# Optimization experiments

Measured on AMD Instinct MI355X. Metric: run time of the kernel, lower is better.

## Reference

```python
import jax, jax.numpy as jnp
import numpy as np

H1 = 51  # lstm1 hidden size
H2 = 1   # lstm2 hidden size


def _lstm_cell(x, h, c, Wih, Whh, bih, bhh):
    # PyTorch LSTMCell: gates = x W_ih^T + b_ih + h W_hh^T + b_hh, order i,f,g,o
    gates = x @ Wih.T + h @ Whh.T + (bih + bhh)
    i, f, g, o = jnp.split(gates, 4, axis=-1)
    i = jax.nn.sigmoid(i)
    f = jax.nn.sigmoid(f)
    g = jnp.tanh(g)
    o = jax.nn.sigmoid(o)
    c_new = f * c + i * g
    h_new = o * jnp.tanh(c_new)
    return h_new, c_new


def setup_inputs() -> dict:
    key = jax.random.key(0)
    ks = jax.random.split(key, 9)
    B, T = 2048, 1024
    s1 = 1.0 / np.sqrt(H1)
    s2 = 1.0 / np.sqrt(H2)
    u = lambda k, shape, s: jax.random.uniform(k, shape, jnp.float32, -s, s)
    return {
        "input": jax.random.normal(ks[0], (B, T), dtype=jnp.float32),
        "W_ih1": u(ks[1], (4 * H1, 1), s1),
        "W_hh1": u(ks[2], (4 * H1, H1), s1),
        "b_ih1": u(ks[3], (4 * H1,), s1),
        "b_hh1": u(ks[4], (4 * H1,), s1),
        "W_ih2": u(ks[5], (4 * H2, H1), s2),
        "W_hh2": u(ks[6], (4 * H2, H2), s2),
        "b_ih2": u(ks[7], (4 * H2,), s2),
        "b_hh2": u(ks[8], (4 * H2,), s2),
        "future": 64,
    }


def reference(input, W_ih1, W_hh1, b_ih1, b_hh1, W_ih2, W_hh2, b_ih2, b_hh2, future):
    B = input.shape[0]
    dt = input.dtype
    h1 = jnp.zeros((B, H1), dt)
    c1 = jnp.zeros((B, H1), dt)
    h2 = jnp.zeros((B, H2), dt)
    c2 = jnp.zeros((B, H2), dt)

    def step(carry, x_t):
        h1, c1, h2, c2 = carry
        h1, c1 = _lstm_cell(x_t, h1, c1, W_ih1, W_hh1, b_ih1, b_hh1)
        h2, c2 = _lstm_cell(h1, h2, c2, W_ih2, W_hh2, b_ih2, b_hh2)
        return (h1, c1, h2, c2), h2

    xs = jnp.swapaxes(input, 0, 1)[:, :, None]  # [T, B, 1]
    carry, outs = jax.lax.scan(step, (h1, c1, h2, c2), xs)

    def step_future(carry, _):
        h1, c1, h2, c2 = carry
        h1, c1 = _lstm_cell(h2, h1, c1, W_ih1, W_hh1, b_ih1, b_hh1)
        h2, c2 = _lstm_cell(h1, h2, c2, W_ih2, W_hh2, b_ih2, b_hh2)
        return (h1, c1, h2, c2), h2

    if future > 0:
        _, outs_f = jax.lax.scan(step_future, carry, None, length=future)
        outs = jnp.concatenate([outs, outs_f], axis=0)

    # [T+F, B, 1] -> [B, T+F]
    return jnp.swapaxes(outs[:, :, 0], 0, 1)
```

## Files before the change

kernel.cpp:

```cpp
#include <hip/hip_runtime.h>


#define H1N  51
#define NP   26
#define NQ   13
#define WAVE 64

typedef float v2f __attribute__((ext_vector_type(2)));
typedef float v4f __attribute__((ext_vector_type(4)));

#define INV_LN2   1.44269504088896340736f
#define INV_LN2X2 2.88539008177792681472f

__device__ __forceinline__ float sigmoid_s(float xs) {
    return __builtin_amdgcn_rcpf(1.0f + __builtin_amdgcn_exp2f(-xs));
}
__device__ __forceinline__ float tanh_s2(float xs2) {
    float e = __builtin_amdgcn_exp2f(xs2);
    return fmaf(-2.0f, __builtin_amdgcn_rcpf(e + 1.0f), 1.0f);
}
__device__ __forceinline__ float tanh_nat(float x) {
    return tanh_s2(x * INV_LN2X2);
}
__device__ __forceinline__ float rdlane(float v, int k) {
    return __int_as_float(__builtin_amdgcn_readlane(__float_as_int(v), k));
}

__global__ __attribute__((amdgpu_flat_work_group_size(128, 128),
                          amdgpu_waves_per_eu(2)))
void lstm_pp(const float* __restrict__ input,
             const float* __restrict__ W_ih1,
             const float* __restrict__ W_hh1,
             const float* __restrict__ b_ih1,
             const float* __restrict__ b_hh1,
             const float* __restrict__ W_ih2,
             const float* __restrict__ W_hh2,
             const float* __restrict__ b_ih2,
             const float* __restrict__ b_hh2,
             float* __restrict__ out,
             int T, int TF)
{
    const int tid = threadIdx.x;
    const int j   = tid & (WAVE - 1);
    const int wid = tid >> 6;
    const bool w0 = (wid == 0);
    const bool jv = (j < H1N);
    const int jj  = jv ? j : 0;
    const float m = jv ? 1.0f : 0.0f;
    const bool isz = (j >= H1N) && (j < H1N + 4);
    const int  q   = isz ? (j - H1N) : 0;
    const float mz  = isz ? 1.0f : 0.0f;
    const float mzA = w0 ? mz : 0.0f;
    const float s2q = (q == 2) ? INV_LN2X2 : INV_LN2;

    const int rA = (w0 ? 0 : 2*H1N)   + jj;
    const int rB = (w0 ? H1N : 3*H1N) + jj;
    const float sclA = w0 ? INV_LN2 : INV_LN2X2;
    const float sclB = INV_LN2;

    __shared__ __align__(16) float hrow[2][2][WAVE];
    __shared__ __align__(16) float xch[2][WAVE][2];
    __shared__ __align__(16) float zbB[4];

    v2f wA[NP], wB[NP];
#pragma unroll
    for (int kk = 0; kk < NP; ++kk) {
        const int k0 = 2*kk, k1 = k0 + 1;
        wA[kk].x = m*sclA*W_hh1[rA*H1N + k0] + mzA*s2q*W_ih2[q*H1N + k0];
        wB[kk].x = m*sclB*W_hh1[rB*H1N + k0];
        if (k1 < H1N) {
            wA[kk].y = m*sclA*W_hh1[rA*H1N + k1] + mzA*s2q*W_ih2[q*H1N + k1];
            wB[kk].y = m*sclB*W_hh1[rB*H1N + k1];
        } else {
            wA[kk].y = m*sclA*(b_ih1[rA] + b_hh1[rA]);
            wB[kk].y = m*sclB*(b_ih1[rB] + b_hh1[rB]);
        }
    }
#pragma unroll
    for (int kk = 0; kk < NP; ++kk)
        asm volatile("" : "+v"(wA[kk]), "+v"(wB[kk]));

    const float wx_i = m*INV_LN2  *W_ih1[jj];
    const float wx_f = m*INV_LN2  *W_ih1[H1N + jj];
    const float wx_g = m*INV_LN2X2*W_ih1[2*H1N + jj];
    const float wx_o = m*INV_LN2  *W_ih1[3*H1N + jj];

    const float wh2_0 = INV_LN2*W_hh2[0], wh2_1 = INV_LN2*W_hh2[1];
    const float wh2_2 = INV_LN2X2*W_hh2[2], wh2_3 = INV_LN2*W_hh2[3];
    const float b2_0 = INV_LN2*(b_ih2[0] + b_hh2[0]), b2_1 = INV_LN2*(b_ih2[1] + b_hh2[1]);
    const float b2_2 = INV_LN2X2*(b_ih2[2] + b_hh2[2]), b2_3 = INV_LN2*(b_ih2[3] + b_hh2[3]);

    {
        const float e = (j == H1N) ? 1.0f : 0.0f;
        if (w0) { hrow[0][0][j] = e; hrow[0][1][j] = e; }
        else    { hrow[1][0][j] = e; hrow[1][1][j] = e; }
    }
    __syncthreads();

    const int myseq = wid;
    const float* __restrict__ xrow = input + (long)(2*blockIdx.x + myseq) * T;
    float* __restrict__ orow = out + (long)(2*blockIdx.x + myseq) * TF;

    float c1 = 0.0f, h2 = 0.0f, c2 = 0.0f, obuf = 0.0f, xbuf = 0.0f;
    float ownA = 0.0f, ownB = 0.0f, rdA = 0.0f, rdB = 0.0f;
    float zA0 = 0.0f, zA1 = 0.0f, zA2 = 0.0f, zA3 = 0.0f;
    float4 zB4 = {0.0f, 0.0f, 0.0f, 0.0f};

    int par = 1;

    auto MV1 = [&](int seq, float& sA_, float& sB_) {
        v2f aA = {0.0f, 0.0f}, aB = {0.0f, 0.0f};
#pragma unroll
        for (int kq = 0; kq < NQ; ++kq) {
            const v4f h4 = *(const v4f*)&hrow[seq][par][4*kq];
            const v2f hp0 = __builtin_shufflevector(h4, h4, 0, 1);
            const v2f hp1 = __builtin_shufflevector(h4, h4, 2, 3);
            asm("v_pk_fma_f32 %0, %2, %4, %0\n\t"
                "v_pk_fma_f32 %1, %3, %4, %1"
                : "+v"(aA), "+v"(aB)
                : "v"(wA[2*kq]), "v"(wB[2*kq]), "v"(hp0));
            asm("v_pk_fma_f32 %0, %2, %4, %0\n\t"
                "v_pk_fma_f32 %1, %3, %4, %1"
                : "+v"(aA), "+v"(aB)
                : "v"(wA[2*kq+1]), "v"(wB[2*kq+1]), "v"(hp1));
        }
        sA_ = aA.x + aA.y;
        sB_ = aB.x + aB.y;
    };

    auto MVX = [&]() {
        float s0A, s0B, s1A, s1B;
        MV1(0, s0A, s0B);
        MV1(1, s1A, s1B);
        v2f pr;
        pr.x = w0 ? s1A : s0A;
        pr.y = w0 ? s1B : s0B;
        *(v2f*)&xch[w0 ? 1 : 0][j][0] = pr;
        if (w0) {
            if (isz) zbB[q] = s1A;
            zA0 = rdlane(s0A, H1N + 0);
            zA1 = rdlane(s0A, H1N + 1);
            zA2 = rdlane(s0A, H1N + 2);
            zA3 = rdlane(s0A, H1N + 3);
        }
        ownA = w0 ? s0A : s1A;
        ownB = w0 ? s0B : s1B;
        __syncthreads();
        const v2f mo = *(const v2f*)&xch[w0 ? 0 : 1][j][0];
        rdA = mo.x; rdB = mo.y;
        if (!w0) zB4 = *(const float4*)zbB;
    };

    auto TAIL = [&](int t, int do_l2, int do_fin, int xmode) {
        const float mI = w0 ? ownA : rdA;
        const float mF = w0 ? ownB : rdB;
        const float mG = w0 ? rdA  : ownA;
        const float mO = w0 ? rdB  : ownB;

        if (do_l2) {
            const float zz0 = w0 ? zA0 : zB4.x;
            const float zz1 = w0 ? zA1 : zB4.y;
            const float zz2 = w0 ? zA2 : zB4.z;
            const float zz3 = w0 ? zA3 : zB4.w;
            const float g2i = sigmoid_s(fmaf(wh2_0, h2, b2_0 + zz0));
            const float g2f = sigmoid_s(fmaf(wh2_1, h2, b2_1 + zz1));
            const float g2g = tanh_s2 (fmaf(wh2_2, h2, b2_2 + zz2));
            const float g2o = sigmoid_s(fmaf(wh2_3, h2, b2_3 + zz3));
            c2 = fmaf(g2f, c2, g2i * g2g);
            h2 = g2o * tanh_nat(c2);
            obuf = (j == ((t - 1) & 63)) ? h2 : obuf;
            if ((t & 63) == 0) orow[t - 64 + j] = obuf;
        }
        if (do_fin) {
            float x;
            if (xmode == 0) {
                if ((t & 63) == 0) xbuf = xrow[t + j];
                x = rdlane(xbuf, t & 63);
            } else {
                x = h2;
            }
            const float gi = sigmoid_s(fmaf(wx_i, x, mI));
            const float gf = sigmoid_s(fmaf(wx_f, x, mF));
            const float gg = tanh_s2 (fmaf(wx_g, x, mG));
            const float go = sigmoid_s(fmaf(wx_o, x, mO));
            c1 = fmaf(gf, c1, gi * gg);
            const float h1 = go * tanh_nat(c1);
            if (jv) hrow[myseq][par][j] = h1;
        }
    };

    MVX(); par ^= 1;

    TAIL(0, 0, 1, 0);
    __syncthreads();
    MVX(); par ^= 1;

    for (int n = 2; n <= T; ++n) {
        TAIL(n - 1, 1, 1, 0);
        __syncthreads();
        MVX(); par ^= 1;
    }

    for (int n = T + 1; n <= TF; ++n) {
        TAIL(n - 1, 1, 1, 1);
        __syncthreads();
        MVX(); par ^= 1;
    }

    TAIL(TF, 1, 0, 1);
}

extern "C" void kernel_launch(void* const* d_in, const int* in_sizes, int n_in,
                              void* d_out, int out_size, void* d_ws, size_t ws_size,
                              hipStream_t stream) {
    const float* input = (const float*)d_in[0];
    const float* W_ih1 = (const float*)d_in[1];
    const float* W_hh1 = (const float*)d_in[2];
    const float* b_ih1 = (const float*)d_in[3];
    const float* b_hh1 = (const float*)d_in[4];
    const float* W_ih2 = (const float*)d_in[5];
    const float* W_hh2 = (const float*)d_in[6];
    const float* b_ih2 = (const float*)d_in[7];
    const float* b_hh2 = (const float*)d_in[8];
    float* out = (float*)d_out;

    const int B  = 2048;
    const int T  = in_sizes[0] / B;
    const int TF = out_size   / B;

    lstm_pp<<<dim3(B / 2), dim3(2 * WAVE), 0, stream>>>(
        input, W_ih1, W_hh1, b_ih1, b_hh1, W_ih2, W_hh2, b_ih2, b_hh2,
        out, T, TF);
}
```

Before: 1.244 ms.

## Split work across four waves per block, one gate-pair wave each

Each block now runs four waves, two per sequence: one wave computes the i/f gate rows and one the g/o rows, each for a single sequence. Before, each of two waves did the matvec for both sequences. Per-wave matvec work per step is halved, and the cross-sequence z exchange goes away. In exchange the g/o waves sit idle during the gate and tail math, block-wide barriers now span four waves, and each block uses twice as many threads, which reduces how many blocks fit per CU.

```diff
diff --git a/kernel.cpp b/kernel.cpp
--- a/kernel.cpp
+++ b/kernel.cpp
@@ -26,9 +26,9 @@
     return __int_as_float(__builtin_amdgcn_readlane(__float_as_int(v), k));
 }
 
-__global__ __attribute__((amdgpu_flat_work_group_size(128, 128),
+__global__ __attribute__((amdgpu_flat_work_group_size(256, 256),
                           amdgpu_waves_per_eu(2)))
-void lstm_pp(const float* __restrict__ input,
+void lstm_q4(const float* __restrict__ input,
              const float* __restrict__ W_ih1,
              const float* __restrict__ W_hh1,
              const float* __restrict__ b_ih1,
@@ -43,24 +43,24 @@
     const int tid = threadIdx.x;
     const int j   = tid & (WAVE - 1);
     const int wid = tid >> 6;
-    const bool w0 = (wid == 0);
+    const int myseq = wid >> 1;
+    const bool isIF = ((wid & 1) == 0);
     const bool jv = (j < H1N);
     const int jj  = jv ? j : 0;
     const float m = jv ? 1.0f : 0.0f;
     const bool isz = (j >= H1N) && (j < H1N + 4);
     const int  q   = isz ? (j - H1N) : 0;
     const float mz  = isz ? 1.0f : 0.0f;
-    const float mzA = w0 ? mz : 0.0f;
+    const float mzA = isIF ? mz : 0.0f;
     const float s2q = (q == 2) ? INV_LN2X2 : INV_LN2;
 
-    const int rA = (w0 ? 0 : 2*H1N)   + jj;
-    const int rB = (w0 ? H1N : 3*H1N) + jj;
-    const float sclA = w0 ? INV_LN2 : INV_LN2X2;
+    const int rA = (isIF ? 0 : 2*H1N)   + jj;
+    const int rB = (isIF ? H1N : 3*H1N) + jj;
+    const float sclA = isIF ? INV_LN2 : INV_LN2X2;
     const float sclB = INV_LN2;
 
     __shared__ __align__(16) float hrow[2][2][WAVE];
     __shared__ __align__(16) float xch[2][WAVE][2];
-    __shared__ __align__(16) float zbB[4];
 
     v2f wA[NP], wB[NP];
 #pragma unroll
@@ -90,29 +90,29 @@
     const float b2_0 = INV_LN2*(b_ih2[0] + b_hh2[0]), b2_1 = INV_LN2*(b_ih2[1] + b_hh2[1]);
     const float b2_2 = INV_LN2X2*(b_ih2[2] + b_hh2[2]), b2_3 = INV_LN2*(b_ih2[3] + b_hh2[3]);
 
-    {
+    if (isIF) {
         const float e = (j == H1N) ? 1.0f : 0.0f;
-        if (w0) { hrow[0][0][j] = e; hrow[0][1][j] = e; }
-        else    { hrow[1][0][j] = e; hrow[1][1][j] = e; }
+        hrow[myseq][0][j] = e;
+        hrow[myseq][1][j] = e;
     }
     __syncthreads();
 
-    const int myseq = wid;
-    const float* __restrict__ xrow = input + (long)(2*blockIdx.x + myseq) * T;
-    float* __restrict__ orow = out + (long)(2*blockIdx.x + myseq) * TF;
+    const int s = 2 * blockIdx.x + myseq;
+    const float* __restrict__ xrow = input + (long)s * T;
+    float* __restrict__ orow = out + (long)s * TF;
 
     float c1 = 0.0f, h2 = 0.0f, c2 = 0.0f, obuf = 0.0f, xbuf = 0.0f;
     float ownA = 0.0f, ownB = 0.0f, rdA = 0.0f, rdB = 0.0f;
     float zA0 = 0.0f, zA1 = 0.0f, zA2 = 0.0f, zA3 = 0.0f;
-    float4 zB4 = {0.0f, 0.0f, 0.0f, 0.0f};
 
     int par = 1;
 
-    auto MV1 = [&](int seq, float& sA_, float& sB_) {
+    auto MVX = [&]() {
         v2f aA = {0.0f, 0.0f}, aB = {0.0f, 0.0f};
+        const float* __restrict__ hb = &hrow[myseq][par][0];
 #pragma unroll
         for (int kq = 0; kq < NQ; ++kq) {
-            const v4f h4 = *(const v4f*)&hrow[seq][par][4*kq];
+            const v4f h4 = *(const v4f*)&hb[4*kq];
             const v2f hp0 = __builtin_shufflevector(h4, h4, 0, 1);
             const v2f hp1 = __builtin_shufflevector(h4, h4, 2, 3);
             asm("v_pk_fma_f32 %0, %2, %4, %0\n\t"
@@ -124,48 +124,33 @@
                 : "+v"(aA), "+v"(aB)
                 : "v"(wA[2*kq+1]), "v"(wB[2*kq+1]), "v"(hp1));
         }
-        sA_ = aA.x + aA.y;
-        sB_ = aB.x + aB.y;
+        const float sA_ = aA.x + aA.y;
+        const float sB_ = aB.x + aB.y;
+        if (isIF) {
+            ownA = sA_; ownB = sB_;
+            zA0 = rdlane(sA_, H1N + 0);
+            zA1 = rdlane(sA_, H1N + 1);
+            zA2 = rdlane(sA_, H1N + 2);
+            zA3 = rdlane(sA_, H1N + 3);
+        } else {
+            v2f pr; pr.x = sA_; pr.y = sB_;
+            *(v2f*)&xch[myseq][j][0] = pr;
+        }
+        __syncthreads();
+        if (isIF) {
+            const v2f mo = *(const v2f*)&xch[myseq][j][0];
+            rdA = mo.x; rdB = mo.y;
+        }
     };
 
-    auto MVX = [&]() {
-        float s0A, s0B, s1A, s1B;
-        MV1(0, s0A, s0B);
-        MV1(1, s1A, s1B);
-        v2f pr;
-        pr.x = w0 ? s1A : s0A;
-        pr.y = w0 ? s1B : s0B;
-        *(v2f*)&xch[w0 ? 1 : 0][j][0] = pr;
-        if (w0) {
-            if (isz) zbB[q] = s1A;
-            zA0 = rdlane(s0A, H1N + 0);
-            zA1 = rdlane(s0A, H1N + 1);
-            zA2 = rdlane(s0A, H1N + 2);
-            zA3 = rdlane(s0A, H1N + 3);
-        }
-        ownA = w0 ? s0A : s1A;
-        ownB = w0 ? s0B : s1B;
-        __syncthreads();
-        const v2f mo = *(const v2f*)&xch[w0 ? 0 : 1][j][0];
-        rdA = mo.x; rdB = mo.y;
-        if (!w0) zB4 = *(const float4*)zbB;
-    };
-
     auto TAIL = [&](int t, int do_l2, int do_fin, int xmode) {
-        const float mI = w0 ? ownA : rdA;
-        const float mF = w0 ? ownB : rdB;
-        const float mG = w0 ? rdA  : ownA;
-        const float mO = w0 ? rdB  : ownB;
+        const float mI = ownA, mF = ownB, mG = rdA, mO = rdB;
 
         if (do_l2) {
-            const float zz0 = w0 ? zA0 : zB4.x;
-            const float zz1 = w0 ? zA1 : zB4.y;
-            const float zz2 = w0 ? zA2 : zB4.z;
-            const float zz3 = w0 ? zA3 : zB4.w;
-            const float g2i = sigmoid_s(fmaf(wh2_0, h2, b2_0 + zz0));
-            const float g2f = sigmoid_s(fmaf(wh2_1, h2, b2_1 + zz1));
-            const float g2g = tanh_s2 (fmaf(wh2_2, h2, b2_2 + zz2));
-            const float g2o = sigmoid_s(fmaf(wh2_3, h2, b2_3 + zz3));
+            const float g2i = sigmoid_s(fmaf(wh2_0, h2, b2_0 + zA0));
+            const float g2f = sigmoid_s(fmaf(wh2_1, h2, b2_1 + zA1));
+            const float g2g = tanh_s2 (fmaf(wh2_2, h2, b2_2 + zA2));
+            const float g2o = sigmoid_s(fmaf(wh2_3, h2, b2_3 + zA3));
             c2 = fmaf(g2f, c2, g2i * g2g);
             h2 = g2o * tanh_nat(c2);
             obuf = (j == ((t - 1) & 63)) ? h2 : obuf;
@@ -191,23 +176,23 @@
 
     MVX(); par ^= 1;
 
-    TAIL(0, 0, 1, 0);
+    if (isIF) TAIL(0, 0, 1, 0);
     __syncthreads();
     MVX(); par ^= 1;
 
     for (int n = 2; n <= T; ++n) {
-        TAIL(n - 1, 1, 1, 0);
+        if (isIF) TAIL(n - 1, 1, 1, 0);
         __syncthreads();
         MVX(); par ^= 1;
     }
 
     for (int n = T + 1; n <= TF; ++n) {
-        TAIL(n - 1, 1, 1, 1);
+        if (isIF) TAIL(n - 1, 1, 1, 1);
         __syncthreads();
         MVX(); par ^= 1;
     }
 
-    TAIL(TF, 1, 0, 1);
+    if (isIF) TAIL(TF, 1, 0, 1);
 }
 
 extern "C" void kernel_launch(void* const* d_in, const int* in_sizes, int n_in,
@@ -228,7 +213,7 @@
     const int T  = in_sizes[0] / B;
     const int TF = out_size   / B;
 
-    lstm_pp<<<dim3(B / 2), dim3(2 * WAVE), 0, stream>>>(
+    lstm_q4<<<dim3(B / 2), dim3(4 * WAVE), 0, stream>>>(
         input, W_ih1, W_hh1, b_ih1, b_hh1, W_ih2, W_hh2, b_ih2, b_hh2,
         out, T, TF);
 }
```

After: 1.377 ms. 10.7% more time.
